# Performance work log

Measured on AMD Instinct MI355X. Metric: run time of the kernel, lower is better.

Reference implementation:

```python
import jax, jax.numpy as jnp
import numpy as np

N = 50000
P = 200000
L = 6
IN_DIM = 128
OUT_DIM = 128
HEADS = 4


def setup_inputs() -> dict:
    key = jax.random.key(0)
    ks = jax.random.split(key, 7)
    x = jax.random.normal(ks[0], (N, IN_DIM), dtype=jnp.float32)
    path_list = jax.random.randint(ks[1], (P, L), 0, N, dtype=jnp.int64)
    s = 0.1
    w_ih = jax.random.normal(ks[2], (3 * OUT_DIM, IN_DIM), dtype=jnp.float32) * s
    w_hh = jax.random.normal(ks[3], (3 * OUT_DIM, OUT_DIM), dtype=jnp.float32) * s
    b_ih = jax.random.normal(ks[4], (3 * OUT_DIM,), dtype=jnp.float32) * s
    b_hh = jax.random.normal(ks[5], (3 * OUT_DIM,), dtype=jnp.float32) * s
    a = jax.random.uniform(ks[6], (OUT_DIM, HEADS), dtype=jnp.float32) * 2.0 - 1.0
    return {"x": x, "path_list": path_list, "w_ih": w_ih, "w_hh": w_hh,
            "b_ih": b_ih, "b_hh": b_hh, "a": a}


def _gru_final_hidden(feats, w_ih, w_hh, b_ih, b_hh):
    # feats: [P, L, in_dim]; PyTorch GRU cell semantics, h0 = 0.
    out_dim = w_hh.shape[1]
    p = feats.shape[0]

    def step(h, xt):
        gi = xt @ w_ih.T + b_ih          # [P, 3*out]
        gh = h @ w_hh.T + b_hh           # [P, 3*out]
        ir, iz, i_n = jnp.split(gi, 3, axis=-1)
        hr, hz, h_n = jnp.split(gh, 3, axis=-1)
        r = jax.nn.sigmoid(ir + hr)
        z = jax.nn.sigmoid(iz + hz)
        n_cand = jnp.tanh(i_n + r * h_n)
        h_new = (1.0 - z) * n_cand + z * h
        return h_new, None

    h0 = jnp.zeros((p, out_dim), feats.dtype)
    xs = jnp.swapaxes(feats, 0, 1)       # [L, P, in_dim]
    h, _ = jax.lax.scan(step, h0, xs)
    return h                              # [P, out_dim]


def reference(x, path_list, w_ih, w_hh, b_ih, b_hh, a):
    n, out_dim = x.shape[0], w_hh.shape[1]
    heads = a.shape[1]
    # F.embedding(path_list, x): gather path features [P, L, in_dim]
    feats = x[path_list]
    path_emb = _gru_final_hidden(feats, w_ih, w_hh, b_ih, b_hh)       # [P, out]
    # unnormalized attention per head
    att_un = jnp.exp(jax.nn.leaky_relu(path_emb @ a, negative_slope=0.2))  # [P, H]
    row = path_list[:, -1]                                             # owner node of each path
    # M @ att_un : segment-sum over owner nodes
    att_sum = jax.ops.segment_sum(att_un, row, num_segments=n)         # [N, H]
    # M.t() @ (1/att_sum) : gather back to paths
    att_low = (1.0 / att_sum)[row]                                     # [P, H]
    att_n = att_un * att_low                                           # [P, H]
    # reshape(-1,1).repeat(1,out).reshape(P,-1): each head's scalar repeated out_dim times
    att_rep = jnp.repeat(att_n, out_dim, axis=1)                       # [P, H*out]
    emb_rep = jnp.tile(path_emb, (1, heads))                           # [P, H*out]
    path_att_emb = att_rep * emb_rep
    node_att_emb = jax.ops.segment_sum(path_att_emb, row, num_segments=n)  # [N, H*out]
    return node_att_emb
```

## Files before the change

kernel.cpp:

```cpp
#include <hip/hip_runtime.h>
#include <hip/hip_bf16.h>
#include <math.h>

#define NN 50000
#define PP 200000
#define LL 6
#define DD 128
#define HH 4

#define TM 64
#define NT 512
#define HPAD 132

typedef __attribute__((ext_vector_type(8))) short short8;
typedef __attribute__((ext_vector_type(4))) float f32x4;

__device__ __forceinline__ unsigned short f2bf(float v) {
    __hip_bfloat16 h = __float2bfloat16(v);
    return *(unsigned short*)&h;
}
__device__ __forceinline__ float bf2f(unsigned short u) {
    union { unsigned int i; float f; } c; c.i = ((unsigned int)u) << 16; return c.f;
}
__device__ __forceinline__ float fast_rcp(float x) { return __builtin_amdgcn_rcpf(x); }
__device__ __forceinline__ float fast_sigmoid(float x) {
    return fast_rcp(1.f + __expf(-x));
}
__device__ __forceinline__ float fast_tanh(float x) {
    float e = __expf(-2.f * fabsf(x));
    float t = (1.f - e) * fast_rcp(1.f + e);
    return copysignf(t, x);
}

__global__ void prep_w_kernel(const float* __restrict__ w_hh,
                              unsigned short* __restrict__ whb) {
    int i = blockIdx.x * 256 + threadIdx.x;
    if (i < 3 * DD * DD) whb[i] = f2bf(w_hh[i]);
}

__global__ void histo_kernel(const int* __restrict__ path_list,
                             int* __restrict__ cnt) {
    int p = blockIdx.x * 256 + threadIdx.x;
    if (p < PP) atomicAdd(&cnt[path_list[p * LL + (LL - 1)]], 1);
}

__global__ void scan_kernel(const int* __restrict__ cnt,
                            int* __restrict__ offs,
                            int* __restrict__ cursor) {
    __shared__ int ls[256];
    const int t = threadIdx.x;
    const int chunk = (NN + 255) / 256;
    int s = 0;
    for (int j = 0; j < chunk; ++j) {
        int i = t + j * 256;
        if (i < NN) s += cnt[i];
    }
    ls[t] = s; __syncthreads();
    for (int off = 1; off < 256; off <<= 1) {
        int v = (t >= off) ? ls[t - off] : 0;
        __syncthreads();
        ls[t] += v;
        __syncthreads();
    }
    int run = (t == 0) ? 0 : ls[t - 1];
    for (int j = 0; j < chunk; ++j) {
        int i = t + j * 256;
        if (i < NN) { offs[i] = run; cursor[i] = run; run += cnt[i]; }
    }
}

__global__ void scatter_kernel(const int* __restrict__ path_list,
                               int* __restrict__ cursor,
                               int* __restrict__ sorted) {
    int p = blockIdx.x * 256 + threadIdx.x;
    if (p < PP) {
        int row = path_list[p * LL + (LL - 1)];
        int k = atomicAdd(&cursor[row], 1);
        sorted[k] = p;
    }
}

__global__ __launch_bounds__(512, 2)
void gi_gemm_kernel(const float* __restrict__ x,
                    const float* __restrict__ w_ih,
                    const float* __restrict__ b_ih,
                    const float* __restrict__ b_hh,
                    float* __restrict__ gi)
{
    const int tid  = threadIdx.x;
    const int lane = tid & 63;
    const int wave = tid >> 6;
    const int lcol = lane & 15;
    const int quad = lane >> 4;
    const int ko   = quad * 8;
    const int r0   = blockIdx.x * 64;

    short8 B[3][4];
    float bias[3];
    #pragma unroll
    for (int j = 0; j < 3; ++j) {
        int col = wave * 48 + j * 16 + lcol;
        #pragma unroll
        for (int ks = 0; ks < 4; ++ks) {
            const float* src = w_ih + (size_t)col * 128 + ks * 32 + ko;
            short8 b;
            #pragma unroll
            for (int e = 0; e < 8; ++e) b[e] = (short)f2bf(src[e]);
            B[j][ks] = b;
        }
        bias[j] = b_ih[col] + ((col < 256) ? b_hh[col] : 0.f);
    }

    f32x4 acc[3][4];
    #pragma unroll
    for (int j = 0; j < 3; ++j)
        #pragma unroll
        for (int rt = 0; rt < 4; ++rt)
            acc[j][rt] = (f32x4){bias[j], bias[j], bias[j], bias[j]};

    #pragma unroll
    for (int ks = 0; ks < 4; ++ks) {
        #pragma unroll
        for (int rt = 0; rt < 4; ++rt) {
            int row = r0 + rt * 16 + lcol;
            if (row >= NN) row = NN - 1;
            const float* src = x + (size_t)row * 128 + ks * 32 + ko;
            short8 av;
            #pragma unroll
            for (int e = 0; e < 8; ++e) av[e] = (short)f2bf(src[e]);
            acc[0][rt] = __builtin_amdgcn_mfma_f32_16x16x32_bf16(av, B[0][ks], acc[0][rt], 0, 0, 0);
            acc[1][rt] = __builtin_amdgcn_mfma_f32_16x16x32_bf16(av, B[1][ks], acc[1][rt], 0, 0, 0);
            acc[2][rt] = __builtin_amdgcn_mfma_f32_16x16x32_bf16(av, B[2][ks], acc[2][rt], 0, 0, 0);
        }
    }

    #pragma unroll
    for (int j = 0; j < 3; ++j) {
        int col = wave * 48 + j * 16 + lcol;
        #pragma unroll
        for (int rt = 0; rt < 4; ++rt)
            #pragma unroll
            for (int rr = 0; rr < 4; ++rr) {
                int row = r0 + rt * 16 + quad * 4 + rr;
                if (row < NN) gi[(size_t)row * 384 + col] = acc[j][rt][rr];
            }
    }
}

__global__ __launch_bounds__(NT, 2)
void gru_att_kernel(const float* __restrict__ gi,
                    const int*   __restrict__ path_list,
                    const unsigned short* __restrict__ whb,
                    const float* __restrict__ b_hh,
                    const float* __restrict__ a,
                    float* __restrict__ att_sum,
                    unsigned short* __restrict__ emb,
                    float* __restrict__ att_un_g)
{
    __shared__ __align__(16) unsigned char smem[43520];
    unsigned short* hsb0   = (unsigned short*)smem;
    unsigned short* hsb1   = (unsigned short*)(smem + 16384);
    float*          hs_f   = (float*)smem;
    float*          red_s  = (float*)(smem + 33792);
    int*            nodes_s= (int*)(smem + 41984);

    const int tid  = threadIdx.x;
    const int lane = tid & 63;
    const int wave = tid >> 6;
    const int lcol = lane & 15;
    const int quad = lane >> 4;
    const int d    = wave * 16 + lcol;
    const int p0   = blockIdx.x * TM;
    const int ko   = quad * 8;

    short8 Bh[3][4];
    #pragma unroll
    for (int c = 0; c < 3; ++c)
        #pragma unroll
        for (int ks = 0; ks < 4; ++ks)
            Bh[c][ks] = *(const short8*)(whb + (size_t)(c * DD + d) * DD + ks * 32 + ko);
    const float bhn = b_hh[d + 256];

    for (int i = tid; i < TM * LL; i += NT) nodes_s[i] = path_list[(size_t)p0 * LL + i];
    for (int i = tid; i < TM * DD / 8; i += NT)
        ((uint4*)hsb0)[i] = make_uint4(0u, 0u, 0u, 0u);

    float hreg[16];
    #pragma unroll
    for (int i = 0; i < 16; ++i) hreg[i] = 0.f;

    __syncthreads();

    for (int t = 0; t < LL; ++t) {
        unsigned short* hr = (t & 1) ? hsb1 : hsb0;
        unsigned short* hw = (t & 1) ? hsb0 : hsb1;

        float gin[16];
        f32x4 accR[4], accZ[4], accH[4];
        #pragma unroll
        for (int rt = 0; rt < 4; ++rt)
            #pragma unroll
            for (int r = 0; r < 4; ++r) {
                const int p = rt * 16 + quad * 4 + r;
                const int node = nodes_s[p * LL + t];
                const float* g = gi + (size_t)node * 384 + d;
                accR[rt][r] = g[0];
                accZ[rt][r] = g[128];
                gin[rt * 4 + r] = g[256];
            }
        #pragma unroll
        for (int rt = 0; rt < 4; ++rt)
            accH[rt] = (f32x4){bhn, bhn, bhn, bhn};

        #pragma unroll
        for (int ks = 0; ks < 4; ++ks) {
            const int kb = ks * 4 + quad;
            #pragma unroll
            for (int rt = 0; rt < 4; ++rt) {
                const int p = rt * 16 + lcol;
                short8 ah = *(const short8*)(hr + p * DD + ((kb ^ lcol) * 8));
                accR[rt] = __builtin_amdgcn_mfma_f32_16x16x32_bf16(ah, Bh[0][ks], accR[rt], 0, 0, 0);
                accZ[rt] = __builtin_amdgcn_mfma_f32_16x16x32_bf16(ah, Bh[1][ks], accZ[rt], 0, 0, 0);
                accH[rt] = __builtin_amdgcn_mfma_f32_16x16x32_bf16(ah, Bh[2][ks], accH[rt], 0, 0, 0);
            }
        }

        if (t == LL - 1) __syncthreads();

        #pragma unroll
        for (int rt = 0; rt < 4; ++rt) {
            #pragma unroll
            for (int r = 0; r < 4; ++r) {
                const int idx = rt * 4 + r;
                const int p   = rt * 16 + quad * 4 + r;
                float rg = fast_sigmoid(accR[rt][r]);
                float zg = fast_sigmoid(accZ[rt][r]);
                float ng = fast_tanh(gin[idx] + rg * accH[rt][r]);
                float hnew = fmaf(zg, hreg[idx] - ng, ng);
                hreg[idx] = hnew;
                if (t < LL - 1) {
                    hw[p * DD + (((d >> 3) ^ (p & 15)) * 8) + (d & 7)] = f2bf(hnew);
                } else {
                    hs_f[p * HPAD + d] = hnew;
                }
            }
        }
        __syncthreads();
    }

    {
        int pi = tid >> 3, tt = tid & 7;
        float s0 = 0.f, s1 = 0.f, s2 = 0.f, s3 = 0.f;
        unsigned short pack[16];
        #pragma unroll
        for (int j = 0; j < 16; ++j) {
            int dd2 = tt * 16 + j;
            float hv = hs_f[pi * HPAD + dd2];
            pack[j] = f2bf(hv);
            float4 av = *(const float4*)(a + dd2 * 4);
            s0 += hv * av.x; s1 += hv * av.y; s2 += hv * av.z; s3 += hv * av.w;
        }
        uint4* dst = (uint4*)(emb + (size_t)(p0 + pi) * DD + tt * 16);
        dst[0] = *(uint4*)&pack[0];
        dst[1] = *(uint4*)&pack[8];
        float* rp = red_s + (pi * 8 + tt) * 4;
        rp[0] = s0; rp[1] = s1; rp[2] = s2; rp[3] = s3;
    }
    __syncthreads();
    if (tid < TM) {
        int pi = tid;
        int row = nodes_s[pi * LL + (LL - 1)];
        float4 e4;
        #pragma unroll
        for (int h = 0; h < HH; ++h) {
            float s = 0.f;
            #pragma unroll
            for (int tt = 0; tt < 8; ++tt) s += red_s[(pi * 8 + tt) * 4 + h];
            float lv = (s > 0.f) ? s : 0.2f * s;
            float e  = __expf(lv);
            ((float*)&e4)[h] = e;
            atomicAdd(&att_sum[row * HH + h], e);
        }
        *(float4*)(att_un_g + (size_t)(p0 + pi) * HH) = e4;
    }
}

__global__ __launch_bounds__(256)
void agg_kernel(const unsigned short* __restrict__ emb,
                const float* __restrict__ att_un,
                const float* __restrict__ att_sum,
                const int* __restrict__ offs,
                const int* __restrict__ cnt,
                const int* __restrict__ sorted,
                float* __restrict__ out)
{
    int node = blockIdx.x * 2 + (threadIdx.x >> 7);
    int d    = threadIdx.x & 127;
    if (node >= NN) return;
    int start = offs[node];
    int len   = cnt[node];
    float a0 = 0.f, a1 = 0.f, a2 = 0.f, a3 = 0.f;
    for (int i = 0; i < len; ++i) {
        int p = sorted[start + i];
        float4 at = *(const float4*)(att_un + (size_t)p * 4);
        float ev = bf2f(emb[(size_t)p * DD + d]);
        a0 = fmaf(at.x, ev, a0);
        a1 = fmaf(at.y, ev, a1);
        a2 = fmaf(at.z, ev, a2);
        a3 = fmaf(at.w, ev, a3);
    }
    float4 s = *(const float4*)(att_sum + (size_t)node * 4);
    float* o = out + (size_t)node * 512 + d;
    o[0]   = (s.x > 0.f) ? a0 / s.x : 0.f;
    o[128] = (s.y > 0.f) ? a1 / s.y : 0.f;
    o[256] = (s.z > 0.f) ? a2 / s.z : 0.f;
    o[384] = (s.w > 0.f) ? a3 / s.w : 0.f;
}

extern "C" void kernel_launch(void* const* d_in, const int* in_sizes, int n_in,
                              void* d_out, int out_size, void* d_ws, size_t ws_size,
                              hipStream_t stream) {
    const float* x         = (const float*)d_in[0];
    const int*   path_list = (const int*)  d_in[1];
    const float* w_ih      = (const float*)d_in[2];
    const float* w_hh      = (const float*)d_in[3];
    const float* b_ih      = (const float*)d_in[4];
    const float* b_hh      = (const float*)d_in[5];
    const float* a         = (const float*)d_in[6];
    float* out = (float*)d_out;

    char* w = (char*)d_ws;
    float*          att_sum = (float*)w;                 w += 800000;
    int*            cnt     = (int*)w;                   w += 200000;
    int*            offs    = (int*)w;                   w += 200000;
    int*            cursor  = (int*)w;                   w += 200000;
    int*            sorted  = (int*)w;                   w += 800000;
    float*          att_un  = (float*)w;                 w += 3200000;
    float*          gi      = (float*)w;                 w += 76800000;
    unsigned short* whb     = (unsigned short*)w;        w += 98304;
    unsigned short* emb     = (unsigned short*)w;        w += 51200000;

    hipMemsetAsync(att_sum, 0, 800000, stream);
    hipMemsetAsync(cnt, 0, 200000, stream);

    prep_w_kernel<<<(3 * DD * DD + 255) / 256, 256, 0, stream>>>(w_hh, whb);

    histo_kernel<<<(PP + 255) / 256, 256, 0, stream>>>(path_list, cnt);
    scan_kernel<<<1, 256, 0, stream>>>(cnt, offs, cursor);
    scatter_kernel<<<(PP + 255) / 256, 256, 0, stream>>>(path_list, cursor, sorted);

    gi_gemm_kernel<<<(NN + 63) / 64, 512, 0, stream>>>(x, w_ih, b_ih, b_hh, gi);

    gru_att_kernel<<<PP / TM, NT, 0, stream>>>(gi, path_list, whb,
                                               b_hh, a, att_sum, emb, att_un);

    agg_kernel<<<(NN + 1) / 2, 256, 0, stream>>>(emb, att_un, att_sum,
                                                 offs, cnt, sorted, out);
}
```

Baseline: 724.8 us.

## Interleave gate projections per column, halve GRU path tile, raise occupancy

The gi precompute now stores the r, z and n gate values for each hidden column next to each other, so the GRU kernel can fetch all three with one contiguous 12-byte read per node instead of three reads 512 bytes apart. The x and w_ih loads in the projection GEMM become float4 vector loads. The GRU kernel's path tile shrinks from 64 to 32, with smaller shared memory and launch bounds raised to 4 blocks per CU, to increase occupancy and hide the gather latency. In exchange, the recurrent weight fragments are reloaded by twice as many blocks, and the interleaved stores in the GEMM are strided and less coalesced.

```diff
diff --git a/kernel.cpp b/kernel.cpp
--- a/kernel.cpp
+++ b/kernel.cpp
@@ -8,12 +8,14 @@
 #define DD 128
 #define HH 4
 
-#define TM 64
+#define TM 32
 #define NT 512
 #define HPAD 132
 
 typedef __attribute__((ext_vector_type(8))) short short8;
 typedef __attribute__((ext_vector_type(4))) float f32x4;
+
+struct f3 { float x, y, z; };
 
 __device__ __forceinline__ unsigned short f2bf(float v) {
     __hip_bfloat16 h = __float2bfloat16(v);
@@ -93,30 +95,34 @@
     const int lcol = lane & 15;
     const int quad = lane >> 4;
     const int ko   = quad * 8;
+    const int d    = wave * 16 + lcol;
     const int r0   = blockIdx.x * 64;
 
     short8 B[3][4];
     float bias[3];
     #pragma unroll
-    for (int j = 0; j < 3; ++j) {
-        int col = wave * 48 + j * 16 + lcol;
+    for (int c = 0; c < 3; ++c) {
+        int col = c * 128 + d;
         #pragma unroll
         for (int ks = 0; ks < 4; ++ks) {
-            const float* src = w_ih + (size_t)col * 128 + ks * 32 + ko;
+            const float4* src = (const float4*)(w_ih + (size_t)col * 128 + ks * 32 + ko);
+            float4 f0 = src[0], f1 = src[1];
             short8 b;
-            #pragma unroll
-            for (int e = 0; e < 8; ++e) b[e] = (short)f2bf(src[e]);
-            B[j][ks] = b;
-        }
-        bias[j] = b_ih[col] + ((col < 256) ? b_hh[col] : 0.f);
+            b[0] = (short)f2bf(f0.x); b[1] = (short)f2bf(f0.y);
+            b[2] = (short)f2bf(f0.z); b[3] = (short)f2bf(f0.w);
+            b[4] = (short)f2bf(f1.x); b[5] = (short)f2bf(f1.y);
+            b[6] = (short)f2bf(f1.z); b[7] = (short)f2bf(f1.w);
+            B[c][ks] = b;
+        }
+        bias[c] = b_ih[col] + ((c < 2) ? b_hh[col] : 0.f);
     }
 
     f32x4 acc[3][4];
     #pragma unroll
-    for (int j = 0; j < 3; ++j)
+    for (int c = 0; c < 3; ++c)
         #pragma unroll
         for (int rt = 0; rt < 4; ++rt)
-            acc[j][rt] = (f32x4){bias[j], bias[j], bias[j], bias[j]};
+            acc[c][rt] = (f32x4){bias[c], bias[c], bias[c], bias[c]};
 
     #pragma unroll
     for (int ks = 0; ks < 4; ++ks) {
@@ -124,10 +130,13 @@
         for (int rt = 0; rt < 4; ++rt) {
             int row = r0 + rt * 16 + lcol;
             if (row >= NN) row = NN - 1;
-            const float* src = x + (size_t)row * 128 + ks * 32 + ko;
+            const float4* src = (const float4*)(x + (size_t)row * 128 + ks * 32 + ko);
+            float4 f0 = src[0], f1 = src[1];
             short8 av;
-            #pragma unroll
-            for (int e = 0; e < 8; ++e) av[e] = (short)f2bf(src[e]);
+            av[0] = (short)f2bf(f0.x); av[1] = (short)f2bf(f0.y);
+            av[2] = (short)f2bf(f0.z); av[3] = (short)f2bf(f0.w);
+            av[4] = (short)f2bf(f1.x); av[5] = (short)f2bf(f1.y);
+            av[6] = (short)f2bf(f1.z); av[7] = (short)f2bf(f1.w);
             acc[0][rt] = __builtin_amdgcn_mfma_f32_16x16x32_bf16(av, B[0][ks], acc[0][rt], 0, 0, 0);
             acc[1][rt] = __builtin_amdgcn_mfma_f32_16x16x32_bf16(av, B[1][ks], acc[1][rt], 0, 0, 0);
             acc[2][rt] = __builtin_amdgcn_mfma_f32_16x16x32_bf16(av, B[2][ks], acc[2][rt], 0, 0, 0);
@@ -135,19 +144,20 @@
     }
 
     #pragma unroll
-    for (int j = 0; j < 3; ++j) {
-        int col = wave * 48 + j * 16 + lcol;
-        #pragma unroll
-        for (int rt = 0; rt < 4; ++rt)
-            #pragma unroll
-            for (int rr = 0; rr < 4; ++rr) {
-                int row = r0 + rt * 16 + quad * 4 + rr;
-                if (row < NN) gi[(size_t)row * 384 + col] = acc[j][rt][rr];
+    for (int rt = 0; rt < 4; ++rt)
+        #pragma unroll
+        for (int rr = 0; rr < 4; ++rr) {
+            int row = r0 + rt * 16 + quad * 4 + rr;
+            if (row < NN) {
+                float* o = gi + (size_t)row * 384 + d * 3;
+                o[0] = acc[0][rt][rr];
+                o[1] = acc[1][rt][rr];
+                o[2] = acc[2][rt][rr];
             }
-    }
-}
-
-__global__ __launch_bounds__(NT, 2)
+        }
+}
+
+__global__ __launch_bounds__(NT, 4)
 void gru_att_kernel(const float* __restrict__ gi,
                     const int*   __restrict__ path_list,
                     const unsigned short* __restrict__ whb,
@@ -157,12 +167,12 @@
                     unsigned short* __restrict__ emb,
                     float* __restrict__ att_un_g)
 {
-    __shared__ __align__(16) unsigned char smem[43520];
-    unsigned short* hsb0   = (unsigned short*)smem;
-    unsigned short* hsb1   = (unsigned short*)(smem + 16384);
+    __shared__ __align__(16) unsigned char smem[25856];
+    unsigned short* hs0    = (unsigned short*)smem;
+    unsigned short* hs1    = (unsigned short*)(smem + 8192);
     float*          hs_f   = (float*)smem;
-    float*          red_s  = (float*)(smem + 33792);
-    int*            nodes_s= (int*)(smem + 41984);
+    float*          red_s  = (float*)(smem + 16896);
+    int*            nodes_s= (int*)(smem + 25088);
 
     const int tid  = threadIdx.x;
     const int lane = tid & 63;
@@ -182,41 +192,42 @@
     const float bhn = b_hh[d + 256];
 
     for (int i = tid; i < TM * LL; i += NT) nodes_s[i] = path_list[(size_t)p0 * LL + i];
-    for (int i = tid; i < TM * DD / 8; i += NT)
-        ((uint4*)hsb0)[i] = make_uint4(0u, 0u, 0u, 0u);
-
-    float hreg[16];
-    #pragma unroll
-    for (int i = 0; i < 16; ++i) hreg[i] = 0.f;
+    if (tid < TM * DD / 8)
+        ((uint4*)hs0)[tid] = make_uint4(0u, 0u, 0u, 0u);
+
+    float hreg[8];
+    #pragma unroll
+    for (int i = 0; i < 8; ++i) hreg[i] = 0.f;
 
     __syncthreads();
 
+    #pragma unroll
     for (int t = 0; t < LL; ++t) {
-        unsigned short* hr = (t & 1) ? hsb1 : hsb0;
-        unsigned short* hw = (t & 1) ? hsb0 : hsb1;
-
-        float gin[16];
-        f32x4 accR[4], accZ[4], accH[4];
-        #pragma unroll
-        for (int rt = 0; rt < 4; ++rt)
+        unsigned short* hr = (t & 1) ? hs1 : hs0;
+        unsigned short* hw = (t & 1) ? hs0 : hs1;
+
+        float gin[8];
+        f32x4 accR[2], accZ[2], accH[2];
+        #pragma unroll
+        for (int rt = 0; rt < 2; ++rt)
             #pragma unroll
             for (int r = 0; r < 4; ++r) {
                 const int p = rt * 16 + quad * 4 + r;
                 const int node = nodes_s[p * LL + t];
-                const float* g = gi + (size_t)node * 384 + d;
-                accR[rt][r] = g[0];
-                accZ[rt][r] = g[128];
-                gin[rt * 4 + r] = g[256];
+                f3 g = *(const f3*)(gi + (size_t)node * 384 + d * 3);
+                accR[rt][r] = g.x;
+                accZ[rt][r] = g.y;
+                gin[rt * 4 + r] = g.z;
             }
         #pragma unroll
-        for (int rt = 0; rt < 4; ++rt)
+        for (int rt = 0; rt < 2; ++rt)
             accH[rt] = (f32x4){bhn, bhn, bhn, bhn};
 
         #pragma unroll
         for (int ks = 0; ks < 4; ++ks) {
             const int kb = ks * 4 + quad;
             #pragma unroll
-            for (int rt = 0; rt < 4; ++rt) {
+            for (int rt = 0; rt < 2; ++rt) {
                 const int p = rt * 16 + lcol;
                 short8 ah = *(const short8*)(hr + p * DD + ((kb ^ lcol) * 8));
                 accR[rt] = __builtin_amdgcn_mfma_f32_16x16x32_bf16(ah, Bh[0][ks], accR[rt], 0, 0, 0);
@@ -228,7 +239,7 @@
         if (t == LL - 1) __syncthreads();
 
         #pragma unroll
-        for (int rt = 0; rt < 4; ++rt) {
+        for (int rt = 0; rt < 2; ++rt) {
             #pragma unroll
             for (int r = 0; r < 4; ++r) {
                 const int idx = rt * 4 + r;
@@ -249,21 +260,19 @@
     }
 
     {
-        int pi = tid >> 3, tt = tid & 7;
+        int pi = tid >> 4, tt = tid & 15;
         float s0 = 0.f, s1 = 0.f, s2 = 0.f, s3 = 0.f;
-        unsigned short pack[16];
-        #pragma unroll
-        for (int j = 0; j < 16; ++j) {
-            int dd2 = tt * 16 + j;
+        unsigned short pack[8];
+        #pragma unroll
+        for (int j = 0; j < 8; ++j) {
+            int dd2 = tt * 8 + j;
             float hv = hs_f[pi * HPAD + dd2];
             pack[j] = f2bf(hv);
             float4 av = *(const float4*)(a + dd2 * 4);
             s0 += hv * av.x; s1 += hv * av.y; s2 += hv * av.z; s3 += hv * av.w;
         }
-        uint4* dst = (uint4*)(emb + (size_t)(p0 + pi) * DD + tt * 16);
-        dst[0] = *(uint4*)&pack[0];
-        dst[1] = *(uint4*)&pack[8];
-        float* rp = red_s + (pi * 8 + tt) * 4;
+        *(uint4*)(emb + (size_t)(p0 + pi) * DD + tt * 8) = *(uint4*)&pack[0];
+        float* rp = red_s + (pi * 16 + tt) * 4;
         rp[0] = s0; rp[1] = s1; rp[2] = s2; rp[3] = s3;
     }
     __syncthreads();
@@ -275,7 +284,7 @@
         for (int h = 0; h < HH; ++h) {
             float s = 0.f;
             #pragma unroll
-            for (int tt = 0; tt < 8; ++tt) s += red_s[(pi * 8 + tt) * 4 + h];
+            for (int tt = 0; tt < 16; ++tt) s += red_s[(pi * 16 + tt) * 4 + h];
             float lv = (s > 0.f) ? s : 0.2f * s;
             float e  = __expf(lv);
             ((float*)&e4)[h] = e;
```

Result: slower. 1.068 ms (+47.4%).

## Interleave gi gate columns and prefetch next timestep's gathered gates

Applied to the files above, without the earlier changes.

The input-gate GEMM now writes r, z and n values for each hidden unit contiguously (stride 3), so the GRU kernel gathers one 12-byte record per path row instead of three scattered floats. The GRU loop software-pipelines these gathers, issuing loads for step t+1 before the recurrent MFMAs of step t so global latency overlaps with compute. Weight and x loads become float4 vector loads. Barriers are replaced with an LDS-only wait plus s_barrier, which avoids waiting on the in-flight global prefetches but raises register pressure.

```diff
diff --git a/kernel.cpp b/kernel.cpp
--- a/kernel.cpp
+++ b/kernel.cpp
@@ -14,6 +14,8 @@
 
 typedef __attribute__((ext_vector_type(8))) short short8;
 typedef __attribute__((ext_vector_type(4))) float f32x4;
+
+struct f3 { float x, y, z; };
 
 __device__ __forceinline__ unsigned short f2bf(float v) {
     __hip_bfloat16 h = __float2bfloat16(v);
@@ -93,30 +95,34 @@
     const int lcol = lane & 15;
     const int quad = lane >> 4;
     const int ko   = quad * 8;
+    const int d    = wave * 16 + lcol;
     const int r0   = blockIdx.x * 64;
 
     short8 B[3][4];
     float bias[3];
     #pragma unroll
-    for (int j = 0; j < 3; ++j) {
-        int col = wave * 48 + j * 16 + lcol;
+    for (int c = 0; c < 3; ++c) {
+        int col = c * 128 + d;
         #pragma unroll
         for (int ks = 0; ks < 4; ++ks) {
-            const float* src = w_ih + (size_t)col * 128 + ks * 32 + ko;
+            const float4* src = (const float4*)(w_ih + (size_t)col * 128 + ks * 32 + ko);
+            float4 f0 = src[0], f1 = src[1];
             short8 b;
-            #pragma unroll
-            for (int e = 0; e < 8; ++e) b[e] = (short)f2bf(src[e]);
-            B[j][ks] = b;
-        }
-        bias[j] = b_ih[col] + ((col < 256) ? b_hh[col] : 0.f);
+            b[0] = (short)f2bf(f0.x); b[1] = (short)f2bf(f0.y);
+            b[2] = (short)f2bf(f0.z); b[3] = (short)f2bf(f0.w);
+            b[4] = (short)f2bf(f1.x); b[5] = (short)f2bf(f1.y);
+            b[6] = (short)f2bf(f1.z); b[7] = (short)f2bf(f1.w);
+            B[c][ks] = b;
+        }
+        bias[c] = b_ih[col] + ((c < 2) ? b_hh[col] : 0.f);
     }
 
     f32x4 acc[3][4];
     #pragma unroll
-    for (int j = 0; j < 3; ++j)
+    for (int c = 0; c < 3; ++c)
         #pragma unroll
         for (int rt = 0; rt < 4; ++rt)
-            acc[j][rt] = (f32x4){bias[j], bias[j], bias[j], bias[j]};
+            acc[c][rt] = (f32x4){bias[c], bias[c], bias[c], bias[c]};
 
     #pragma unroll
     for (int ks = 0; ks < 4; ++ks) {
@@ -124,10 +130,13 @@
         for (int rt = 0; rt < 4; ++rt) {
             int row = r0 + rt * 16 + lcol;
             if (row >= NN) row = NN - 1;
-            const float* src = x + (size_t)row * 128 + ks * 32 + ko;
+            const float4* src = (const float4*)(x + (size_t)row * 128 + ks * 32 + ko);
+            float4 f0 = src[0], f1 = src[1];
             short8 av;
-            #pragma unroll
-            for (int e = 0; e < 8; ++e) av[e] = (short)f2bf(src[e]);
+            av[0] = (short)f2bf(f0.x); av[1] = (short)f2bf(f0.y);
+            av[2] = (short)f2bf(f0.z); av[3] = (short)f2bf(f0.w);
+            av[4] = (short)f2bf(f1.x); av[5] = (short)f2bf(f1.y);
+            av[6] = (short)f2bf(f1.z); av[7] = (short)f2bf(f1.w);
             acc[0][rt] = __builtin_amdgcn_mfma_f32_16x16x32_bf16(av, B[0][ks], acc[0][rt], 0, 0, 0);
             acc[1][rt] = __builtin_amdgcn_mfma_f32_16x16x32_bf16(av, B[1][ks], acc[1][rt], 0, 0, 0);
             acc[2][rt] = __builtin_amdgcn_mfma_f32_16x16x32_bf16(av, B[2][ks], acc[2][rt], 0, 0, 0);
@@ -135,16 +144,17 @@
     }
 
     #pragma unroll
-    for (int j = 0; j < 3; ++j) {
-        int col = wave * 48 + j * 16 + lcol;
-        #pragma unroll
-        for (int rt = 0; rt < 4; ++rt)
-            #pragma unroll
-            for (int rr = 0; rr < 4; ++rr) {
-                int row = r0 + rt * 16 + quad * 4 + rr;
-                if (row < NN) gi[(size_t)row * 384 + col] = acc[j][rt][rr];
+    for (int rt = 0; rt < 4; ++rt)
+        #pragma unroll
+        for (int rr = 0; rr < 4; ++rr) {
+            int row = r0 + rt * 16 + quad * 4 + rr;
+            if (row < NN) {
+                float* o = gi + (size_t)row * 384 + d * 3;
+                o[0] = acc[0][rt][rr];
+                o[1] = acc[1][rt][rr];
+                o[2] = acc[2][rt][rr];
             }
-    }
+        }
 }
 
 __global__ __launch_bounds__(NT, 2)
@@ -158,8 +168,8 @@
                     float* __restrict__ att_un_g)
 {
     __shared__ __align__(16) unsigned char smem[43520];
-    unsigned short* hsb0   = (unsigned short*)smem;
-    unsigned short* hsb1   = (unsigned short*)(smem + 16384);
+    unsigned short* hs0    = (unsigned short*)smem;
+    unsigned short* hs1    = (unsigned short*)(smem + 16384);
     float*          hs_f   = (float*)smem;
     float*          red_s  = (float*)(smem + 33792);
     int*            nodes_s= (int*)(smem + 41984);
@@ -183,7 +193,7 @@
 
     for (int i = tid; i < TM * LL; i += NT) nodes_s[i] = path_list[(size_t)p0 * LL + i];
     for (int i = tid; i < TM * DD / 8; i += NT)
-        ((uint4*)hsb0)[i] = make_uint4(0u, 0u, 0u, 0u);
+        ((uint4*)hs0)[i] = make_uint4(0u, 0u, 0u, 0u);
 
     float hreg[16];
     #pragma unroll
@@ -191,26 +201,45 @@
 
     __syncthreads();
 
+    f3 g[16];
+    #pragma unroll
+    for (int rt = 0; rt < 4; ++rt)
+        #pragma unroll
+        for (int r = 0; r < 4; ++r) {
+            const int p = rt * 16 + quad * 4 + r;
+            const int node = nodes_s[p * LL + 0];
+            g[rt * 4 + r] = *(const f3*)(gi + (size_t)node * 384 + d * 3);
+        }
+
+    #pragma unroll 1
     for (int t = 0; t < LL; ++t) {
-        unsigned short* hr = (t & 1) ? hsb1 : hsb0;
-        unsigned short* hw = (t & 1) ? hsb0 : hsb1;
+        unsigned short* hr = (t & 1) ? hs1 : hs0;
+        unsigned short* hw = (t & 1) ? hs0 : hs1;
 
         float gin[16];
         f32x4 accR[4], accZ[4], accH[4];
         #pragma unroll
-        for (int rt = 0; rt < 4; ++rt)
+        for (int rt = 0; rt < 4; ++rt) {
             #pragma unroll
             for (int r = 0; r < 4; ++r) {
-                const int p = rt * 16 + quad * 4 + r;
-                const int node = nodes_s[p * LL + t];
-                const float* g = gi + (size_t)node * 384 + d;
-                accR[rt][r] = g[0];
-                accZ[rt][r] = g[128];
-                gin[rt * 4 + r] = g[256];
+                const int idx = rt * 4 + r;
+                accR[rt][r] = g[idx].x;
+                accZ[rt][r] = g[idx].y;
+                gin[idx]    = g[idx].z;
             }
-        #pragma unroll
-        for (int rt = 0; rt < 4; ++rt)
             accH[rt] = (f32x4){bhn, bhn, bhn, bhn};
+        }
+
+        if (t < LL - 1) {
+            #pragma unroll
+            for (int rt = 0; rt < 4; ++rt)
+                #pragma unroll
+                for (int r = 0; r < 4; ++r) {
+                    const int p = rt * 16 + quad * 4 + r;
+                    const int node = nodes_s[p * LL + t + 1];
+                    g[rt * 4 + r] = *(const f3*)(gi + (size_t)node * 384 + d * 3);
+                }
+        }
 
         #pragma unroll
         for (int ks = 0; ks < 4; ++ks) {
@@ -225,7 +254,10 @@
             }
         }
 
-        if (t == LL - 1) __syncthreads();
+        if (t == LL - 1) {
+            asm volatile("s_waitcnt lgkmcnt(0)" ::: "memory");
+            __builtin_amdgcn_s_barrier();
+        }
 
         #pragma unroll
         for (int rt = 0; rt < 4; ++rt) {
@@ -245,8 +277,11 @@
                 }
             }
         }
-        __syncthreads();
-    }
+        asm volatile("s_waitcnt lgkmcnt(0)" ::: "memory");
+        __builtin_amdgcn_s_barrier();
+    }
+
+    __syncthreads();
 
     {
         int pi = tid >> 3, tt = tid & 7;
```

Result: slower. 917.1 us (+26.5%).
